# Kernel tuning notes

Hardware: AMD Instinct MI355X
Metric: run time of the kernel (lower is better)

## Reference

```python
import jax, jax.numpy as jnp
import numpy as np

Q_STAGES = 8      # residual VQ stages
K_CODES = 1024    # codebook size per stage
D = 256           # code dim == encoder channels


def setup_inputs() -> dict:
    key = jax.random.key(0)
    ks = jax.random.split(key, 6)
    B, T = 8, 8192
    x = jax.random.normal(ks[0], (B, 1, T), dtype=jnp.float32)
    enc_w = jax.random.normal(ks[1], (D, 1, 3), dtype=jnp.float32) * 0.3
    enc_b = jnp.zeros((D,), dtype=jnp.float32)
    dec_w = jax.random.normal(ks[2], (1, D, 3), dtype=jnp.float32) * (1.0 / np.sqrt(3 * D))
    dec_b = jnp.zeros((1,), dtype=jnp.float32)
    codebooks = jax.random.normal(ks[3], (Q_STAGES, K_CODES, D), dtype=jnp.float32)
    return {"x": x, "enc_w": enc_w, "enc_b": enc_b,
            "dec_w": dec_w, "dec_b": dec_b, "codebooks": codebooks}


def _conv1d(x, w, b):
    # x: [B,C,T], w: [O,I,3], 'same' padding
    y = jax.lax.conv_general_dilated(x, w, window_strides=(1,), padding='SAME',
                                     dimension_numbers=('NCH', 'OIH', 'NCH'))
    return y + b[None, :, None]


def _rvq(z, codebooks):
    # z: [B,D,T] -> tokens [N,D]
    B, d, T = z.shape
    flat = jnp.transpose(z, (0, 2, 1)).reshape(B * T, d)  # [N,D]

    def stage(carry, cb):
        residual, quant_sum, loss = carry
        r2 = jnp.sum(residual * residual, axis=1, keepdims=True)      # [N,1]
        c2 = jnp.sum(cb * cb, axis=1)                                  # [K]
        dist = r2 - 2.0 * (residual @ cb.T) + c2[None, :]              # [N,K]
        idx = jnp.argmin(dist, axis=1)                                 # [N]
        q = jax.lax.stop_gradient(cb[idx])                             # [N,D]
        loss = loss + jnp.mean((residual - q) ** 2)                    # commitment
        return (residual - q, quant_sum + q, loss), None

    init = (flat, jnp.zeros_like(flat), jnp.float32(0.0))
    (res, quant_sum, loss), _ = jax.lax.scan(stage, init, codebooks)
    # straight-through estimator
    quant = flat + jax.lax.stop_gradient(quant_sum - flat)
    quant = jnp.transpose(quant.reshape(B, T, d), (0, 2, 1))           # [B,D,T]
    return quant, loss


def reference(x, enc_w, enc_b, dec_w, dec_b, codebooks):
    encoded = _conv1d(x, enc_w, enc_b)              # [B,256,T]
    quantized, commit_loss = _rvq(encoded, codebooks)
    decoded = _conv1d(quantized, dec_w, dec_b)      # [B,1,T]
    return decoded, commit_loss
```

## Files before the change

kernel.cpp:

```cpp
#include <hip/hip_runtime.h>

#define QS 8
#define KC 1024
#define DD 256
#define TT 8192
#define NN 65536
#define TAU 0.06f

typedef _Float16 half8 __attribute__((ext_vector_type(8)));
typedef float f32x4 __attribute__((ext_vector_type(4)));

__global__ __launch_bounds__(256) void cb_prep_all_kernel(
    const float* __restrict__ cbs, _Float16* __restrict__ cbh)
{
    const int b = blockIdx.x, s = b >> 6, t = b & 63;
    const int cg = t >> 2, kp = t & 3;
    const float* cb = cbs + (size_t)s * KC * DD;
    _Float16* dst = cbh + (size_t)s * KC * DD + (size_t)t * 4096;
    #pragma unroll
    for (int q = 0; q < 2; ++q) {
        const int p = threadIdx.x + 256*q;
        const int kc2 = p >> 8, rem = p & 255;
        const int nt = rem >> 6, l4v = (rem >> 4) & 3, l15v = rem & 15;
        const int code = cg*64 + nt*16 + l15v;
        const int k0 = kp*64 + kc2*32 + l4v*8;
        const float* src = &cb[(long)code*DD + k0];
        const float4 v0 = *reinterpret_cast<const float4*>(src);
        const float4 v1 = *reinterpret_cast<const float4*>(src + 4);
        half8 hv;
        hv[0]=(_Float16)v0.x; hv[1]=(_Float16)v0.y;
        hv[2]=(_Float16)v0.z; hv[3]=(_Float16)v0.w;
        hv[4]=(_Float16)v1.x; hv[5]=(_Float16)v1.y;
        hv[6]=(_Float16)v1.z; hv[7]=(_Float16)v1.w;
        *reinterpret_cast<half8*>(
            &dst[(kc2*4 + nt)*512 + (l4v*16 + l15v)*8]) = hv;
    }
}

__global__ __launch_bounds__(256) void c2_kernel(
    const float* __restrict__ cbs, float* __restrict__ c2,
    float* __restrict__ lossAcc)
{
    if (blockIdx.x == 0 && threadIdx.x == 0) *lossAcc = 0.0f;
    const int w = (int)((blockIdx.x * blockDim.x + threadIdx.x) >> 6);
    const int lane = threadIdx.x & 63;
    if (w >= QS * KC) return;
    const float* row = cbs + (long)w * DD;
    float s = 0.0f;
    #pragma unroll
    for (int q = 0; q < DD / 64; ++q) {
        const float v = row[lane + 64*q];
        s += v * v;
    }
    #pragma unroll
    for (int off = 32; off; off >>= 1) s += __shfl_down(s, off, 64);
    if (lane == 0) c2[w] = s;
}

__global__ __launch_bounds__(512, 3) void mega_kernel(
    const float* __restrict__ x,   const float* __restrict__ ew,
    const float* __restrict__ eb,  const float* __restrict__ cbs,
    const _Float16* __restrict__ cbh, const float* __restrict__ c2all,
    _Float16* __restrict__ resf,   float* __restrict__ lossAcc)
{
    __shared__ __align__(16) _Float16 alds[8 * 512 * 8];
    __shared__ int   idxArr[128];
    __shared__ float rrow[DD];
    __shared__ float sD8[8];
    __shared__ int   sI8[8];
    __shared__ int   flagRows[128];
    __shared__ int   flagCnt;

    const int tid = threadIdx.x;
    const int w   = tid >> 6;
    const int l   = tid & 63;
    const int l15 = l & 15;
    const int l4  = l >> 4;
    const int n0  = blockIdx.x * 128;
    const int n   = n0 + w*16 + l15;

    int tr;
    {
        half8 pa, pb;
        #pragma unroll
        for (int e = 0; e < 8; ++e) {
            pa[e] = (_Float16)l15;
            pb[e] = (_Float16)0.03125f;
        }
        f32x4 pacc = (f32x4){0.f, 0.f, 0.f, 0.f};
        pacc = __builtin_amdgcn_mfma_f32_16x16x32_f16(pa, pb, pacc, 0, 0, 0);
        const float p1 = __shfl(pacc[1], 0, 64);
        tr = (p1 < 0.5f) ? 1 : 0;
    }

    half8 ah[8];
    {
        const int t = n & (TT - 1);
        const float xm = (t > 0)      ? x[n - 1] : 0.0f;
        const float x0v = x[n];
        const float xp = (t < TT - 1) ? x[n + 1] : 0.0f;
        #pragma unroll
        for (int kc = 0; kc < 8; ++kc) {
            half8 hv, lv;
            #pragma unroll
            for (int e = 0; e < 8; ++e) {
                const int d = kc*32 + l4*8 + e;
                const float z = eb[d] + ew[3*d]*xm + ew[3*d+1]*x0v + ew[3*d+2]*xp;
                const _Float16 hh = (_Float16)z;
                hv[e] = hh;
                lv[e] = (_Float16)(z - (float)hh);
            }
            ah[kc] = hv;
            *reinterpret_cast<half8*>(&alds[(kc*512 + tid)*8]) = lv;
        }
    }

    float lsum = 0.0f;

    for (int s = 0; s < QS; ++s) {
        const _Float16* cbhL = cbh + (size_t)s * KC * DD + l*8;
        const float*    cbS  = cbs + (size_t)s * KC * DD;
        const float*    c2S  = c2all + s * KC;

        float b1[4], b2[4]; int i1[4];
        #pragma unroll
        for (int r = 0; r < 4; ++r) { b1[r] = 1e30f; b2[r] = 1e30f; i1[r] = 0; }

        f32x4 acc[4];
        half8 bA[4];

        for (int cg = 0; cg < 16; ++cg) {
            #pragma unroll
            for (int nt = 0; nt < 4; ++nt) acc[nt] = (f32x4){0.f,0.f,0.f,0.f};

            for (int kp = 0; kp < 4; ++kp) {
                const _Float16* base = cbhL + (long)(cg*4 + kp)*4096;
                #pragma unroll
                for (int kc2 = 0; kc2 < 2; ++kc2) {
                    const int kc = kp*2 + kc2;
                    const half8 alv = *reinterpret_cast<const half8*>(
                        &alds[(kc*512 + tid)*8]);
                    #pragma unroll
                    for (int f = 0; f < 4; ++f)
                        bA[f] = *reinterpret_cast<const half8*>(base + (kc2*4 + f)*512);
                    #pragma unroll
                    for (int nt = 0; nt < 4; ++nt) {
                        acc[nt] = __builtin_amdgcn_mfma_f32_16x16x32_f16(ah[kc], bA[nt], acc[nt], 0, 0, 0);
                        acc[nt] = __builtin_amdgcn_mfma_f32_16x16x32_f16(alv,    bA[nt], acc[nt], 0, 0, 0);
                    }
                }
            }

            if (tr == 0) {
                #pragma unroll
                for (int nt = 0; nt < 4; ++nt) {
                    const int code = cg*64 + nt*16 + l15;
                    const float cc = c2S[code];
                    #pragma unroll
                    for (int j = 0; j < 4; ++j) {
                        const float dist = fmaf(-2.0f, acc[nt][j], cc);
                        const bool lt = dist < b1[j];
                        b2[j] = fminf(b2[j], fmaxf(b1[j], dist));
                        b1[j] = lt ? dist : b1[j];
                        i1[j] = lt ? code : i1[j];
                    }
                }
            } else {
                #pragma unroll
                for (int nt = 0; nt < 4; ++nt) {
                    #pragma unroll
                    for (int j = 0; j < 4; ++j) {
                        const int code = cg*64 + nt*16 + l4*4 + j;
                        const float dist = fmaf(-2.0f, acc[nt][j], c2S[code]);
                        const bool lt = dist < b1[0];
                        b2[0] = fminf(b2[0], fmaxf(b1[0], dist));
                        b1[0] = lt ? dist : b1[0];
                        i1[0] = lt ? code : i1[0];
                    }
                }
            }
        }

        __syncthreads();
        if (tid == 0) flagCnt = 0;
        __syncthreads();

        if (tr == 0) {
            #pragma unroll
            for (int m = 1; m < 16; m <<= 1) {
                #pragma unroll
                for (int r = 0; r < 4; ++r) {
                    const float ob1 = __shfl_xor(b1[r], m, 64);
                    const float ob2 = __shfl_xor(b2[r], m, 64);
                    const int   oi1 = __shfl_xor(i1[r], m, 64);
                    const float nb2 = fminf(fminf(b2[r], ob2), fmaxf(b1[r], ob1));
                    if (ob1 < b1[r] || (ob1 == b1[r] && oi1 < i1[r])) { b1[r] = ob1; i1[r] = oi1; }
                    b2[r] = nb2;
                }
            }
            if (l15 == 0) {
                #pragma unroll
                for (int j = 0; j < 4; ++j) {
                    const int row = w*16 + l4*4 + j;
                    idxArr[row] = i1[j];
                    if (b2[j] - b1[j] < TAU) {
                        const int pos = atomicAdd(&flagCnt, 1);
                        flagRows[pos] = row;
                    }
                }
            }
        } else {
            #pragma unroll
            for (int m = 16; m <= 32; m <<= 1) {
                const float ob1 = __shfl_xor(b1[0], m, 64);
                const float ob2 = __shfl_xor(b2[0], m, 64);
                const int   oi1 = __shfl_xor(i1[0], m, 64);
                const float nb2 = fminf(fminf(b2[0], ob2), fmaxf(b1[0], ob1));
                if (ob1 < b1[0] || (ob1 == b1[0] && oi1 < i1[0])) { b1[0] = ob1; i1[0] = oi1; }
                b2[0] = nb2;
            }
            if (l4 == 0) {
                const int row = w*16 + l15;
                idxArr[row] = i1[0];
                if (b2[0] - b1[0] < TAU) {
                    const int pos = atomicAdd(&flagCnt, 1);
                    flagRows[pos] = row;
                }
            }
        }
        __syncthreads();

        const int fc = flagCnt;
        for (int f = 0; f < fc; ++f) {
            const int row = flagRows[f];
            if (w == (row >> 4) && l15 == (row & 15)) {
                #pragma unroll
                for (int kc = 0; kc < 8; ++kc) {
                    const half8 alv = *reinterpret_cast<const half8*>(
                        &alds[(kc*512 + tid)*8]);
                    #pragma unroll
                    for (int e = 0; e < 8; ++e)
                        rrow[kc*32 + l4*8 + e] = (float)ah[kc][e] + (float)alv[e];
                }
            }
            __syncthreads();
            float bd = 1e30f; int bi = 0;
            #pragma unroll
            for (int q = 0; q < 2; ++q) {
                const int code = tid*2 + q;
                const float* crow = cbS + (size_t)code * DD;
                float dot = 0.f;
                for (int d4 = 0; d4 < DD; d4 += 4) {
                    const float4 cv = *reinterpret_cast<const float4*>(&crow[d4]);
                    dot += rrow[d4]*cv.x + rrow[d4+1]*cv.y
                         + rrow[d4+2]*cv.z + rrow[d4+3]*cv.w;
                }
                const float dist = c2S[code] - 2.0f*dot;
                if (dist < bd || (dist == bd && code < bi)) { bd = dist; bi = code; }
            }
            #pragma unroll
            for (int off = 32; off; off >>= 1) {
                const float od = __shfl_down(bd, off, 64);
                const int   oi = __shfl_down(bi, off, 64);
                if (od < bd || (od == bd && oi < bi)) { bd = od; bi = oi; }
            }
            if (l == 0) { sD8[w] = bd; sI8[w] = bi; }
            __syncthreads();
            if (tid == 0) {
                float fbd = sD8[0]; int fbi = sI8[0];
                #pragma unroll
                for (int ww = 1; ww < 8; ++ww) {
                    if (sD8[ww] < fbd || (sD8[ww] == fbd && sI8[ww] < fbi)) {
                        fbd = sD8[ww]; fbi = sI8[ww];
                    }
                }
                idxArr[row] = fbi;
            }
            __syncthreads();
        }

        const int ix = idxArr[w*16 + l15];
        const float* crow = cbS + (size_t)ix * DD;
        #pragma unroll
        for (int kc = 0; kc < 8; ++kc) {
            const float4 c0 = *reinterpret_cast<const float4*>(&crow[kc*32 + l4*8]);
            const float4 c1 = *reinterpret_cast<const float4*>(&crow[kc*32 + l4*8 + 4]);
            const float cv[8] = {c0.x, c0.y, c0.z, c0.w, c1.x, c1.y, c1.z, c1.w};
            const half8 alv = *reinterpret_cast<const half8*>(
                &alds[(kc*512 + tid)*8]);
            half8 hv, lv;
            #pragma unroll
            for (int e = 0; e < 8; ++e) {
                const float rv = ((float)ah[kc][e] + (float)alv[e]) - cv[e];
                lsum += rv * rv;
                const _Float16 hh = (_Float16)rv;
                hv[e] = hh;
                lv[e] = (_Float16)(rv - (float)hh);
            }
            ah[kc] = hv;
            *reinterpret_cast<half8*>(&alds[(kc*512 + tid)*8]) = lv;
        }
    }

    #pragma unroll
    for (int kc = 0; kc < 8; ++kc) {
        const half8 alv = *reinterpret_cast<const half8*>(&alds[(kc*512 + tid)*8]);
        half8 hv;
        #pragma unroll
        for (int e = 0; e < 8; ++e)
            hv[e] = (_Float16)((float)ah[kc][e] + (float)alv[e]);
        *reinterpret_cast<half8*>(&resf[(size_t)n*DD + kc*32 + l4*8]) = hv;
    }
    #pragma unroll
    for (int off = 32; off; off >>= 1) lsum += __shfl_down(lsum, off, 64);
    if (l == 0) atomicAdd(lossAcc, lsum);
}

__global__ __launch_bounds__(256) void decode_kernel(
    const float* __restrict__ x,  const float* __restrict__ ew,
    const float* __restrict__ eb, const _Float16* __restrict__ resf,
    const float* __restrict__ dw, const float* __restrict__ db,
    const float* __restrict__ lossAcc, float* __restrict__ out)
{
    const long n = (long)blockIdx.x * 4 + (threadIdx.x >> 6);
    const int lane = threadIdx.x & 63;
    const int t = (int)(n & (TT - 1));
    float sum = 0.0f;
    #pragma unroll
    for (int k = 0; k < 3; ++k) {
        const int tm = t + k - 1;
        if (tm < 0 || tm > TT - 1) continue;
        const long m = n + k - 1;
        const float xm = (tm > 0)      ? x[m - 1] : 0.0f;
        const float x0 = x[m];
        const float xp = (tm < TT - 1) ? x[m + 1] : 0.0f;
        #pragma unroll
        for (int q = 0; q < 4; ++q) {
            const int d = lane + 64 * q;
            const float z = eb[d] + ew[d*3]*xm + ew[d*3 + 1]*x0 + ew[d*3 + 2]*xp;
            const float quant = z - (float)resf[m * DD + d];
            sum += quant * dw[d*3 + k];
        }
    }
    #pragma unroll
    for (int off = 32; off; off >>= 1) sum += __shfl_down(sum, off, 64);
    if (lane == 0) out[n] = sum + db[0];
    if (blockIdx.x == 0 && threadIdx.x == 0)
        out[NN] = lossAcc[0] * (1.0f / ((float)NN * (float)DD));
}

extern "C" void kernel_launch(void* const* d_in, const int* in_sizes, int n_in,
                              void* d_out, int out_size, void* d_ws, size_t ws_size,
                              hipStream_t stream)
{
    const float* x     = (const float*)d_in[0];
    const float* enc_w = (const float*)d_in[1];
    const float* enc_b = (const float*)d_in[2];
    const float* dec_w = (const float*)d_in[3];
    const float* dec_b = (const float*)d_in[4];
    const float* cbs   = (const float*)d_in[5];
    float* out = (float*)d_out;

    _Float16* resf    = (_Float16*)d_ws;
    _Float16* cbh     = resf + (size_t)NN * DD;
    float*    lossAcc = (float*)(cbh + (size_t)QS * KC * DD);
    float*    c2      = out + 8;

    hipLaunchKernelGGL(cb_prep_all_kernel, dim3(QS * 64), dim3(256), 0, stream,
                       cbs, cbh);
    hipLaunchKernelGGL(c2_kernel, dim3(QS * KC / 4), dim3(256), 0, stream,
                       cbs, c2, lossAcc);
    hipLaunchKernelGGL(mega_kernel, dim3(NN / 128), dim3(512), 0, stream,
                       x, enc_w, enc_b, cbs, cbh, c2, resf, lossAcc);
    hipLaunchKernelGGL(decode_kernel, dim3(NN / 4), dim3(256), 0, stream,
                       x, enc_w, enc_b, resf, dec_w, dec_b, lossAcc, out);
}
```

Baseline: 1.489 ms.

## Split codebook search across two wave halves per 64-row block

Each block now handles 64 rows instead of 128, with two groups of four waves each scanning half of the 1024 codes. The two halves merge their top-2 candidates through shared memory before the tie check and fallback. The grid doubles and the launch-bounds occupancy hint rises to 8, aiming at more waves per CU and better latency hiding. In exchange, each codebook tile is read by twice as many blocks, the residual update runs redundantly in both halves, and extra __syncthreads barriers are added per stage.

```diff
diff --git a/kernel.cpp b/kernel.cpp
--- a/kernel.cpp
+++ b/kernel.cpp
@@ -57,27 +57,31 @@
     if (lane == 0) c2[w] = s;
 }
 
-__global__ __launch_bounds__(512, 3) void mega_kernel(
+__global__ __launch_bounds__(512, 8) void mega_kernel(
     const float* __restrict__ x,   const float* __restrict__ ew,
     const float* __restrict__ eb,  const float* __restrict__ cbs,
     const _Float16* __restrict__ cbh, const float* __restrict__ c2all,
     _Float16* __restrict__ resf,   float* __restrict__ lossAcc)
 {
-    __shared__ __align__(16) _Float16 alds[8 * 512 * 8];
-    __shared__ int   idxArr[128];
+    __shared__ __align__(16) _Float16 alds[4 * 8 * 64 * 8];
+    __shared__ int   idxArr[64];
     __shared__ float rrow[DD];
     __shared__ float sD8[8];
     __shared__ int   sI8[8];
-    __shared__ int   flagRows[128];
+    __shared__ int   flagRows[64];
     __shared__ int   flagCnt;
+    __shared__ float mD1[64], mD2[64];
+    __shared__ int   mI[64];
 
     const int tid = threadIdx.x;
     const int w   = tid >> 6;
+    const int g   = w & 3;
+    const int h   = w >> 2;
     const int l   = tid & 63;
     const int l15 = l & 15;
     const int l4  = l >> 4;
-    const int n0  = blockIdx.x * 128;
-    const int n   = n0 + w*16 + l15;
+    const int n0  = blockIdx.x * 64;
+    const int n   = n0 + g*16 + l15;
 
     int tr;
     {
@@ -111,9 +115,11 @@
                 lv[e] = (_Float16)(z - (float)hh);
             }
             ah[kc] = hv;
-            *reinterpret_cast<half8*>(&alds[(kc*512 + tid)*8]) = lv;
-        }
-    }
+            if (h == 0)
+                *reinterpret_cast<half8*>(&alds[((g*8 + kc)*64 + l)*8]) = lv;
+        }
+    }
+    __syncthreads();
 
     float lsum = 0.0f;
 
@@ -129,7 +135,8 @@
         f32x4 acc[4];
         half8 bA[4];
 
-        for (int cg = 0; cg < 16; ++cg) {
+        for (int cgi = 0; cgi < 8; ++cgi) {
+            const int cg = h*8 + cgi;
             #pragma unroll
             for (int nt = 0; nt < 4; ++nt) acc[nt] = (f32x4){0.f,0.f,0.f,0.f};
 
@@ -139,7 +146,7 @@
                 for (int kc2 = 0; kc2 < 2; ++kc2) {
                     const int kc = kp*2 + kc2;
                     const half8 alv = *reinterpret_cast<const half8*>(
-                        &alds[(kc*512 + tid)*8]);
+                        &alds[((g*8 + kc)*64 + l)*8]);
                     #pragma unroll
                     for (int f = 0; f < 4; ++f)
                         bA[f] = *reinterpret_cast<const half8*>(base + (kc2*4 + f)*512);
@@ -198,15 +205,11 @@
                     b2[r] = nb2;
                 }
             }
-            if (l15 == 0) {
+            if (h == 1 && l15 == 0) {
                 #pragma unroll
                 for (int j = 0; j < 4; ++j) {
-                    const int row = w*16 + l4*4 + j;
-                    idxArr[row] = i1[j];
-                    if (b2[j] - b1[j] < TAU) {
-                        const int pos = atomicAdd(&flagCnt, 1);
-                        flagRows[pos] = row;
-                    }
+                    const int row = g*16 + l4*4 + j;
+                    mD1[row] = b1[j]; mD2[row] = b2[j]; mI[row] = i1[j];
                 }
             }
         } else {
@@ -219,10 +222,42 @@
                 if (ob1 < b1[0] || (ob1 == b1[0] && oi1 < i1[0])) { b1[0] = ob1; i1[0] = oi1; }
                 b2[0] = nb2;
             }
-            if (l4 == 0) {
-                const int row = w*16 + l15;
-                idxArr[row] = i1[0];
-                if (b2[0] - b1[0] < TAU) {
+            if (h == 1 && l4 == 0) {
+                const int row = g*16 + l15;
+                mD1[row] = b1[0]; mD2[row] = b2[0]; mI[row] = i1[0];
+            }
+        }
+        __syncthreads();
+
+        if (tr == 0) {
+            if (h == 0 && l15 == 0) {
+                #pragma unroll
+                for (int j = 0; j < 4; ++j) {
+                    const int row = g*16 + l4*4 + j;
+                    const float d1b = mD1[row], d2b = mD2[row];
+                    const int   ib  = mI[row];
+                    const float nb2 = fminf(fminf(b2[j], d2b), fmaxf(b1[j], d1b));
+                    float nb1; int ni;
+                    if (d1b < b1[j]) { nb1 = d1b; ni = ib; }
+                    else             { nb1 = b1[j]; ni = i1[j]; }
+                    idxArr[row] = ni;
+                    if (nb2 - nb1 < TAU) {
+                        const int pos = atomicAdd(&flagCnt, 1);
+                        flagRows[pos] = row;
+                    }
+                }
+            }
+        } else {
+            if (h == 0 && l4 == 0) {
+                const int row = g*16 + l15;
+                const float d1b = mD1[row], d2b = mD2[row];
+                const int   ib  = mI[row];
+                const float nb2 = fminf(fminf(b2[0], d2b), fmaxf(b1[0], d1b));
+                float nb1; int ni;
+                if (d1b < b1[0]) { nb1 = d1b; ni = ib; }
+                else             { nb1 = b1[0]; ni = i1[0]; }
+                idxArr[row] = ni;
+                if (nb2 - nb1 < TAU) {
                     const int pos = atomicAdd(&flagCnt, 1);
                     flagRows[pos] = row;
                 }
@@ -233,11 +268,11 @@
         const int fc = flagCnt;
         for (int f = 0; f < fc; ++f) {
             const int row = flagRows[f];
-            if (w == (row >> 4) && l15 == (row & 15)) {
+            if (h == 0 && g == (row >> 4) && l15 == (row & 15)) {
                 #pragma unroll
                 for (int kc = 0; kc < 8; ++kc) {
                     const half8 alv = *reinterpret_cast<const half8*>(
-                        &alds[(kc*512 + tid)*8]);
+                        &alds[((g*8 + kc)*64 + l)*8]);
                     #pragma unroll
                     for (int e = 0; e < 8; ++e)
                         rrow[kc*32 + l4*8 + e] = (float)ah[kc][e] + (float)alv[e];
@@ -279,41 +314,51 @@
             __syncthreads();
         }
 
-        const int ix = idxArr[w*16 + l15];
+        half8 alold[8];
+        #pragma unroll
+        for (int kc = 0; kc < 8; ++kc)
+            alold[kc] = *reinterpret_cast<const half8*>(
+                &alds[((g*8 + kc)*64 + l)*8]);
+        __syncthreads();
+
+        const int ix = idxArr[g*16 + l15];
         const float* crow = cbS + (size_t)ix * DD;
         #pragma unroll
         for (int kc = 0; kc < 8; ++kc) {
             const float4 c0 = *reinterpret_cast<const float4*>(&crow[kc*32 + l4*8]);
             const float4 c1 = *reinterpret_cast<const float4*>(&crow[kc*32 + l4*8 + 4]);
             const float cv[8] = {c0.x, c0.y, c0.z, c0.w, c1.x, c1.y, c1.z, c1.w};
-            const half8 alv = *reinterpret_cast<const half8*>(
-                &alds[(kc*512 + tid)*8]);
             half8 hv, lv;
             #pragma unroll
             for (int e = 0; e < 8; ++e) {
-                const float rv = ((float)ah[kc][e] + (float)alv[e]) - cv[e];
-                lsum += rv * rv;
+                const float rv = ((float)ah[kc][e] + (float)alold[kc][e]) - cv[e];
+                if (h == 0) lsum += rv * rv;
                 const _Float16 hh = (_Float16)rv;
                 hv[e] = hh;
                 lv[e] = (_Float16)(rv - (float)hh);
             }
             ah[kc] = hv;
-            *reinterpret_cast<half8*>(&alds[(kc*512 + tid)*8]) = lv;
-        }
-    }
-
-    #pragma unroll
-    for (int kc = 0; kc < 8; ++kc) {
-        const half8 alv = *reinterpret_cast<const half8*>(&alds[(kc*512 + tid)*8]);
-        half8 hv;
-        #pragma unroll
-        for (int e = 0; e < 8; ++e)
-            hv[e] = (_Float16)((float)ah[kc][e] + (float)alv[e]);
-        *reinterpret_cast<half8*>(&resf[(size_t)n*DD + kc*32 + l4*8]) = hv;
-    }
-    #pragma unroll
-    for (int off = 32; off; off >>= 1) lsum += __shfl_down(lsum, off, 64);
-    if (l == 0) atomicAdd(lossAcc, lsum);
+            if (h == 0)
+                *reinterpret_cast<half8*>(&alds[((g*8 + kc)*64 + l)*8]) = lv;
+        }
+        __syncthreads();
+    }
+
+    if (h == 0) {
+        #pragma unroll
+        for (int kc = 0; kc < 8; ++kc) {
+            const half8 alv = *reinterpret_cast<const half8*>(
+                &alds[((g*8 + kc)*64 + l)*8]);
+            half8 hv;
+            #pragma unroll
+            for (int e = 0; e < 8; ++e)
+                hv[e] = (_Float16)((float)ah[kc][e] + (float)alv[e]);
+            *reinterpret_cast<half8*>(&resf[(size_t)n*DD + kc*32 + l4*8]) = hv;
+        }
+        #pragma unroll
+        for (int off = 32; off; off >>= 1) lsum += __shfl_down(lsum, off, 64);
+        if (l == 0) atomicAdd(lossAcc, lsum);
+    }
 }
 
 __global__ __launch_bounds__(256) void decode_kernel(
@@ -370,7 +415,7 @@
                        cbs, cbh);
     hipLaunchKernelGGL(c2_kernel, dim3(QS * KC / 4), dim3(256), 0, stream,
                        cbs, c2, lossAcc);
-    hipLaunchKernelGGL(mega_kernel, dim3(NN / 128), dim3(512), 0, stream,
+    hipLaunchKernelGGL(mega_kernel, dim3(NN / 64), dim3(512), 0, stream,
                        x, enc_w, enc_b, cbs, cbh, c2, resf, lossAcc);
     hipLaunchKernelGGL(decode_kernel, dim3(NN / 4), dim3(256), 0, stream,
                        x, enc_w, enc_b, resf, dec_w, dec_b, lossAcc, out);
```

Result: slower. 3.078 ms (+106.6%).
